# Kernel tuning notes

Hardware: AMD Instinct MI355X
Metric: run time of the kernel (lower is better)

## Reference

```python
import jax, jax.numpy as jnp
import numpy as np


def setup_inputs() -> dict:
    key = jax.random.key(0)
    ks = jax.random.split(key, 12)
    B, L, N, C, Ct, H, RH1, RH2, S = 64, 64, 256, 8, 4, 128, 128, 64, 4
    def rn(k, shape, s=0.08):
        return jax.random.normal(k, shape, dtype=jnp.float32) * s
    return dict(
        x=jax.random.normal(ks[0], (B, L, N, C * Ct), dtype=jnp.float32),
        hidden_intensity=jax.random.normal(ks[1], (B, N, H), dtype=jnp.float32),
        r=jax.random.normal(ks[2], (B, S), dtype=jnp.float32),
        W_ih=rn(ks[3], (4 * H, C)), W_hh=rn(ks[4], (4 * H, H)),
        b_ih=jnp.zeros((4 * H,), jnp.float32), b_hh=jnp.zeros((4 * H,), jnp.float32),
        W1=rn(ks[5], (RH1, 2 * H + 1)), b1=jnp.zeros((RH1,), jnp.float32),
        W2=rn(ks[6], (RH2, RH1)), b2=jnp.zeros((RH2,), jnp.float32),
        W3=rn(ks[7], (C, RH2)), b3=jnp.zeros((C,), jnp.float32),
        Wf=rn(ks[8], (1, C)), bf=jnp.zeros((1,), jnp.float32),
    )


def reference(x, hidden_intensity, r, W_ih, W_hh, b_ih, b_hh,
              W1, b1, W2, b2, W3, b3, Wf, bf):
    # Faithful to torch: nn.LSTM has batch_first=False but is fed (B, L, C),
    # so B is the sequence axis, L the batch axis, and lstm_out[:, -1, :]
    # writes predictions into that last column, so only x[:, -1] matters.
    B, L, N, _ = x.shape
    C = W_ih.shape[1]
    Ct = x.shape[3] // C
    H = W_hh.shape[1]

    def lstm_all_times(seq):  # seq: (T, Bb, C) -> hidden at every time (T, Bb, H)
        xp = jnp.einsum('tbc,gc->tbg', seq, W_ih) + b_ih + b_hh  # (T, Bb, 4H)
        def step(carry, xt):
            h, c = carry
            g = xt + h @ W_hh.T
            i, f, gg, o = jnp.split(g, 4, axis=-1)  # torch gate order i,f,g,o
            c = jax.nn.sigmoid(f) * c + jax.nn.sigmoid(i) * jnp.tanh(gg)
            h = jax.nn.sigmoid(o) * jnp.tanh(c)
            return (h, c), h
        z0 = jnp.zeros((seq.shape[1], H), seq.dtype)
        _, hs = jax.lax.scan(step, (z0, z0), xp)
        return hs

    hi = jnp.broadcast_to(hidden_intensity[:, :, None, :], (B, N, Ct, H))

    def roll(last_col, rj):  # last_col: (B, N, Ct, C), rj: (B,)
        hs = lstm_all_times(last_col.reshape(B, N * Ct, C)).reshape(B, N, Ct, H)
        rr = jnp.broadcast_to(rj[:, None, None, None], (B, N, Ct, 1))
        z = jnp.concatenate([hs, hi, rr], axis=-1)       # (B, N, Ct, 2H+1)
        h1 = jax.nn.relu(z @ W1.T + b1)
        h2 = jax.nn.relu(h1 @ W2.T + b2)
        pr = h2 @ W3.T + b3                              # (B, N, Ct, C)
        contrib = (jax.nn.relu(pr) @ Wf.T + bf)[..., 0].sum(axis=2)  # (B, N)
        return pr, contrib

    last0 = x[:, -1, :, :].reshape(B, N, Ct, C)
    _, preds = jax.lax.scan(roll, last0, r.T)  # (S, B, N)
    return jnp.transpose(preds, (1, 2, 0))     # (B, N, steps_ahead)
```

## Files before the change

kernel.cpp:

```cpp
#include <hip/hip_runtime.h>
#include <hip/hip_bf16.h>


typedef __attribute__((ext_vector_type(8))) _Float16 half8;
typedef __attribute__((ext_vector_type(4))) float f32x4;

#define MFMAH(a, b, c) __builtin_amdgcn_mfma_f32_16x16x32_f16(a, b, c, 0, 0, 0)

__device__ __forceinline__ float sigf(float x)   { return 1.0f / (1.0f + __expf(-x)); }
__device__ __forceinline__ float tanh_f(float x) { return 1.0f - 2.0f / (__expf(2.0f * x) + 1.0f); }

__global__ void prep_k(const float* __restrict__ hi,
                       const float* __restrict__ W1, const float* __restrict__ W2,
                       const float* __restrict__ W3, const float* __restrict__ W_hh,
                       const float* __restrict__ W_ih,
                       _Float16* __restrict__ hi16, _Float16* __restrict__ wp1,
                       _Float16* __restrict__ wp2, _Float16* __restrict__ wp3,
                       _Float16* __restrict__ wpB)
{
    int i = blockIdx.x * 256 + threadIdx.x;
    if (i < 262144) {
        int e = i * 8;
        half8 v;
#pragma unroll
        for (int k = 0; k < 8; ++k) v[k] = (_Float16)hi[e + k];
        *(half8*)(hi16 + e) = v;
        return;
    }
    i -= 262144;
    if (i < 36864) {
        int fragid = i >> 9, lj = i & 511;
        int kt = fragid >> 3, nt = fragid & 7;
        int l = lj >> 3, j = lj & 7;
        int klocal = (l >> 4) * 8 + j;
        int o = nt * 16 + (l & 15);
        float v;
        if (kt < 8)      v = W1[o * 257 + kt * 32 + klocal];
        else             v = (klocal == 0) ? W1[o * 257 + 256] : 0.0f;
        wp1[i] = (_Float16)v;
        return;
    }
    i -= 36864;
    if (i < 8192) {
        int fragid = i >> 9, lj = i & 511;
        int kt = fragid >> 2, nt = fragid & 3;
        int l = lj >> 3, j = lj & 7;
        int k = kt * 32 + (l >> 4) * 8 + j;
        int o = nt * 16 + (l & 15);
        wp2[i] = (_Float16)W2[o * 128 + k];
        return;
    }
    i -= 8192;
    if (i < 1024) {
        int kt = i >> 9, lj = i & 511;
        int l = lj >> 3, j = lj & 7;
        int k = kt * 32 + (l >> 4) * 8 + j;
        int c = l & 15;
        wp3[i] = (_Float16)((c < 8) ? W3[c * 64 + k] : 0.0f);
        return;
    }
    i -= 1024;
    if (i < 81920) {
        int frag = i >> 9, lj = i & 511;
        int kt = frag >> 5, ntile = frag & 31;
        int l = lj >> 3, j = lj & 7;
        int klocal = (l >> 4) * 8 + j;
        int col = ntile * 16 + (l & 15);
        float v;
        if (kt < 4) v = W_hh[col * 128 + kt * 32 + klocal];
        else        v = (klocal < 8) ? W_ih[col * 8 + klocal] : 0.0f;
        wpB[i] = (_Float16)v;
    }
}

__global__ __launch_bounds__(512, 2) void fused_k(
    const float* __restrict__ x, const _Float16* __restrict__ hi16,
    const float* __restrict__ r, const _Float16* __restrict__ wpB,
    const float* __restrict__ b_ih, const float* __restrict__ b_hh,
    const _Float16* __restrict__ wp1, const _Float16* __restrict__ wp2,
    const _Float16* __restrict__ wp3, const float* __restrict__ b1,
    const float* __restrict__ b2, const float* __restrict__ b3,
    const float* __restrict__ Wf, const float* __restrict__ bfp,
    float* __restrict__ out)
{
    __shared__ __align__(16) _Float16 zone[2][4][640];
    __shared__ __align__(16) _Float16 xz[64][32];
    __shared__ __align__(16) _Float16 hsL[256 * 130];
    __shared__ __align__(16) _Float16 h1L[128 * 132];
    __shared__ __align__(16) _Float16 h2L[128 * 68];

    const int t  = threadIdx.x;
    const int cg = t >> 6, l = t & 63;
    const int li = l & 15, lk = l >> 4;
    const int q0 = blockIdx.x * 4, nblk = blockIdx.x;

    const int gsrc[4] = {1, 0, 2, 3};
    half8 bw[4][5];
#pragma unroll
    for (int g = 0; g < 4; ++g)
#pragma unroll
        for (int kt = 0; kt < 5; ++kt) {
            bw[g][kt] = *(const half8*)(wpB + (size_t)(kt * 32 + gsrc[g] * 8 + cg) * 512 + l * 8);
            asm volatile("" : "+a"(bw[g][kt]));
        }
    f32x4 bs4[4];
#pragma unroll
    for (int g = 0; g < 4; ++g) {
        int gc = gsrc[g] * 128 + cg * 16 + li;
        float bv = b_ih[gc] + b_hh[gc];
        bs4[g] = (f32x4){bv, bv, bv, bv};
    }

    if (t < 256) {
        int step = t >> 2, tt = t & 3;
        const float* src = x + (size_t)step * 524288 + 63 * 8192 + (q0 + tt) * 8;
        half8 v;
#pragma unroll
        for (int k = 0; k < 8; ++k) v[k] = (_Float16)src[k];
        *(half8*)&xz[step][tt * 8] = v;
    }

    const int zpl  = cg >> 1;
    const int jl   = (cg & 1) * 16 + li;
    const int roff = (li & 12) * 40 + lk * 8;
    const int srow = lk * 4;
    const _Float16* xrd = &xz[0][(li >> 2) * 8];
    const f32x4 z4 = (f32x4){0.0f, 0.0f, 0.0f, 0.0f};

    for (int j = 0; j < 4; ++j) {
        for (int i = t; i < 1280; i += 512) ((uint*)zone)[i] = 0;
        float cc = 0.0f;
        __syncthreads();

        f32x4 accx[4];
        {
            half8 xa0 = *(const half8*)(xrd);
#pragma unroll
            for (int g = 0; g < 4; ++g)
                accx[g] = MFMAH(xa0, bw[g][4], bs4[g]);
        }

        auto dostep = [&](int step, int p) {
            const int pn = p ^ 1;
            half8 ah[4];
#pragma unroll
            for (int kt = 0; kt < 4; ++kt)
                ah[kt] = *(const half8*)&zone[p][kt][roff];

            __builtin_amdgcn_s_setprio(1);
            f32x4 a0[4], a1[4];
#pragma unroll
            for (int g = 0; g < 4; ++g) {
                a0[g] = MFMAH(ah[0], bw[g][0], accx[g]);
                a1[g] = MFMAH(ah[2], bw[g][2], z4);
            }
#pragma unroll
            for (int g = 0; g < 4; ++g) {
                a0[g] = MFMAH(ah[1], bw[g][1], a0[g]);
                a1[g] = MFMAH(ah[3], bw[g][3], a1[g]);
            }
            float pf = a0[0][0] + a1[0][0];
            float sf = sigf(pf);
            float pi = a0[1][0] + a1[1][0];
            float pg = a0[2][0] + a1[2][0];
            float po = a0[3][0] + a1[3][0];
            cc = sf * cc + sigf(pi) * tanh_f(pg);
            float hv = sigf(po) * tanh_f(cc);
            __builtin_amdgcn_s_setprio(0);
            _Float16 h16 = (_Float16)hv;
            zone[pn][zpl][srow * 40 + jl] = h16;
            hsL[(step * 4 + lk) * 130 + cg * 16 + li] = h16;
            asm volatile("s_waitcnt lgkmcnt(0)\n\ts_barrier" ::: "memory");

            half8 xn = *(const half8*)(xrd + ((step + 1) & 63) * 32);
#pragma unroll
            for (int g = 0; g < 4; ++g)
                accx[g] = MFMAH(xn, bw[g][4], bs4[g]);
        };
        for (int s2 = 0; s2 < 32; ++s2) {
            dostep(s2 * 2,     0);
            dostep(s2 * 2 + 1, 1);
        }

#pragma unroll 1
        for (int p = 0; p < 2; ++p) {
            f32x4 acc[8];
            {
                float bias = b1[cg * 16 + li];
#pragma unroll
                for (int m = 0; m < 8; ++m)
                    acc[m] = (f32x4){bias, bias, bias, bias};
            }
#pragma unroll
            for (int kt = 0; kt < 9; ++kt) {
                half8 bv = *(const half8*)(wp1 + (size_t)(kt * 8 + cg) * 512 + l * 8);
#pragma unroll
                for (int m = 0; m < 8; ++m) {
                    int Mg = p * 8 + m;
                    half8 av;
                    if (kt < 4) {
                        av = *(const half8*)&hsL[(Mg * 16 + li) * 130 + kt * 32 + lk * 8];
                    } else if (kt < 8) {
                        int b = Mg * 4 + (li >> 2);
                        av = *(const half8*)(hi16 + ((size_t)b * 256 + nblk) * 128
                                             + (kt - 4) * 32 + lk * 8);
                    } else {
                        int b = Mg * 4 + (li >> 2);
                        av = (half8){0, 0, 0, 0, 0, 0, 0, 0};
                        if (lk == 0) av[0] = (_Float16)r[b * 4 + j];
                    }
                    acc[m] = MFMAH(av, bv, acc[m]);
                }
            }
#pragma unroll
            for (int m = 0; m < 8; ++m)
#pragma unroll
                for (int reg = 0; reg < 4; ++reg) {
                    float v = fmaxf(acc[m][reg], 0.0f);
                    h1L[(m * 16 + lk * 4 + reg) * 132 + cg * 16 + li] = (_Float16)v;
                }
            __syncthreads();

            {
                const int n2 = cg & 3, mg0 = (cg >> 2) * 4;
                f32x4 acc2[4];
                float bias = b2[n2 * 16 + li];
#pragma unroll
                for (int mi = 0; mi < 4; ++mi)
                    acc2[mi] = (f32x4){bias, bias, bias, bias};
#pragma unroll
                for (int kt = 0; kt < 4; ++kt) {
                    half8 bv = *(const half8*)(wp2 + (size_t)(kt * 4 + n2) * 512 + l * 8);
#pragma unroll
                    for (int mi = 0; mi < 4; ++mi) {
                        int m = mg0 + mi;
                        half8 av = *(const half8*)&h1L[(m * 16 + li) * 132 + kt * 32 + lk * 8];
                        acc2[mi] = MFMAH(av, bv, acc2[mi]);
                    }
                }
#pragma unroll
                for (int mi = 0; mi < 4; ++mi)
#pragma unroll
                    for (int reg = 0; reg < 4; ++reg) {
                        float v = fmaxf(acc2[mi][reg], 0.0f);
                        h2L[((mg0 + mi) * 16 + lk * 4 + reg) * 68 + n2 * 16 + li] = (_Float16)v;
                    }
            }
            __syncthreads();

            {
                f32x4 acc3 = z4;
#pragma unroll
                for (int kt = 0; kt < 2; ++kt) {
                    half8 av = *(const half8*)&h2L[(cg * 16 + li) * 68 + kt * 32 + lk * 8];
                    half8 bv = *(const half8*)(wp3 + (size_t)kt * 512 + l * 8);
                    acc3 = MFMAH(av, bv, acc3);
                }
                const int Mg = p * 8 + cg;
                const int c = li;
                const float b3v = (c < 8) ? b3[c] : 0.0f;
                const float wfv = (c < 8) ? Wf[c] : 0.0f;
                const int b = Mg * 4 + lk;
                float fr[4];
#pragma unroll
                for (int reg = 0; reg < 4; ++reg) {
                    float pr = acc3[reg] + b3v;
                    if (c < 8) xz[b][reg * 8 + c] = (_Float16)pr;
                    fr[reg] = (c < 8) ? fmaxf(pr, 0.0f) * wfv : 0.0f;
                }
#pragma unroll
                for (int reg = 0; reg < 4; ++reg) {
                    fr[reg] += __shfl_xor(fr[reg], 1);
                    fr[reg] += __shfl_xor(fr[reg], 2);
                    fr[reg] += __shfl_xor(fr[reg], 4);
                }
                if (li == 0) {
                    float v = fr[0] + fr[1] + fr[2] + fr[3] + 4.0f * bfp[0];
                    out[((size_t)b * 256 + nblk) * 4 + j] = v;
                }
            }
            __syncthreads();
        }
    }
}

extern "C" void kernel_launch(void* const* d_in, const int* in_sizes, int n_in,
                              void* d_out, int out_size, void* d_ws, size_t ws_size,
                              hipStream_t stream)
{
    const float* x   = (const float*)d_in[0];
    const float* hi  = (const float*)d_in[1];
    const float* r   = (const float*)d_in[2];
    const float* Wih = (const float*)d_in[3];
    const float* Whh = (const float*)d_in[4];
    const float* bih = (const float*)d_in[5];
    const float* bhh = (const float*)d_in[6];
    const float* W1  = (const float*)d_in[7];
    const float* b1  = (const float*)d_in[8];
    const float* W2  = (const float*)d_in[9];
    const float* b2  = (const float*)d_in[10];
    const float* W3  = (const float*)d_in[11];
    const float* b3  = (const float*)d_in[12];
    const float* Wf  = (const float*)d_in[13];
    const float* bf  = (const float*)d_in[14];
    float* out = (float*)d_out;

    _Float16* hi16 = (_Float16*)d_ws;
    _Float16* wp1  = hi16 + 2097152;
    _Float16* wp2  = wp1 + 36864;
    _Float16* wp3  = wp2 + 8192;
    _Float16* wpB  = wp3 + 1024;

    prep_k<<<1524, 256, 0, stream>>>(hi, W1, W2, W3, Whh, Wih,
                                     hi16, wp1, wp2, wp3, wpB);
    fused_k<<<256, 512, 0, stream>>>(x, hi16, r, wpB, bih, bhh,
                                     wp1, wp2, wp3, b1, b2, b3, Wf, bf, out);
}
```

Measured before the change: 281.3 us.

## Wavefront-pipeline the four autoregressive rolls with per-timestep MLP fusion

Result: faster. 253.4 us (-9.9%).

```diff
diff --git a/kernel.cpp b/kernel.cpp
--- a/kernel.cpp
+++ b/kernel.cpp
@@ -84,15 +84,14 @@
     float* __restrict__ out)
 {
     __shared__ __align__(16) _Float16 zone[2][4][640];
-    __shared__ __align__(16) _Float16 xz[64][32];
-    __shared__ __align__(16) _Float16 hsL[256 * 130];
-    __shared__ __align__(16) _Float16 h1L[128 * 132];
-    __shared__ __align__(16) _Float16 h2L[128 * 68];
+    __shared__ __align__(16) _Float16 curA[4][64][32];
+    __shared__ __align__(16) _Float16 h1L[16 * 136];
+    __shared__ __align__(16) _Float16 h2L[16 * 72];
 
     const int t  = threadIdx.x;
     const int cg = t >> 6, l = t & 63;
     const int li = l & 15, lk = l >> 4;
-    const int q0 = blockIdx.x * 4, nblk = blockIdx.x;
+    const int nblk = blockIdx.x, q0 = nblk * 4;
 
     const int gsrc[4] = {1, 0, 2, 3};
     half8 bw[4][5];
@@ -111,176 +110,148 @@
         bs4[g] = (f32x4){bv, bv, bv, bv};
     }
 
+    for (int i = t; i < 2560; i += 512) ((uint*)zone)[i] = 0;
+    for (int i = t; i < 3072; i += 512) ((uint*)&curA[1][0][0])[i] = 0;
     if (t < 256) {
-        int step = t >> 2, tt = t & 3;
-        const float* src = x + (size_t)step * 524288 + 63 * 8192 + (q0 + tt) * 8;
+        int st = t >> 2, tt = t & 3;
+        const float* src = x + (size_t)st * 524288 + 63 * 8192 + (q0 + tt) * 8;
         half8 v;
 #pragma unroll
         for (int k = 0; k < 8; ++k) v[k] = (_Float16)src[k];
-        *(half8*)&xz[step][tt * 8] = v;
-    }
-
-    const int zpl  = cg >> 1;
-    const int jl   = (cg & 1) * 16 + li;
-    const int roff = (li & 12) * 40 + lk * 8;
-    const int srow = lk * 4;
-    const _Float16* xrd = &xz[0][(li >> 2) * 8];
+        *(half8*)&curA[0][st][tt * 8] = v;
+    }
+    float cc[4] = {0.0f, 0.0f, 0.0f, 0.0f};
+    __syncthreads();
+
     const f32x4 z4 = (f32x4){0.0f, 0.0f, 0.0f, 0.0f};
-
-    for (int j = 0; j < 4; ++j) {
-        for (int i = t; i < 1280; i += 512) ((uint*)zone)[i] = 0;
-        float cc = 0.0f;
-        __syncthreads();
-
-        f32x4 accx[4];
+    const int zpl = cg >> 1, jl = (cg & 1) * 16 + li;
+    const int roffL = li * 40 + lk * 8;
+    const int jx = li >> 2, sx = li & 3;
+    const float b1v = b1[cg * 16 + li];
+    const float b2v = (cg < 4) ? b2[cg * 16 + li] : 0.0f;
+    const float b3v = (li < 8) ? b3[li] : 0.0f;
+    const float wfv = (li < 8) ? Wf[li] : 0.0f;
+    const float bfv = bfp[0];
+
+#pragma unroll 1
+    for (int T = 0; T < 67; ++T) {
+        const int p = T & 1, pn = p ^ 1;
+        const int tb = (T - jx) & 63;
+
+        half8 xa = *(const half8*)&curA[jx][tb][sx * 8];
+        half8 ahi[4];
+#pragma unroll
+        for (int kt = 0; kt < 4; ++kt)
+            ahi[kt] = *(const half8*)(hi16 + ((size_t)(tb * 256 + nblk)) * 128
+                                      + kt * 32 + lk * 8);
+        half8 arf = (half8){0, 0, 0, 0, 0, 0, 0, 0};
+        if (lk == 0) arf[0] = (_Float16)r[tb * 4 + jx];
+
+        half8 ah[4];
+#pragma unroll
+        for (int kt = 0; kt < 4; ++kt)
+            ah[kt] = *(const half8*)&zone[p][kt][roffL];
+
+        f32x4 a0[4], a1[4];
+#pragma unroll
+        for (int g = 0; g < 4; ++g)
+            a0[g] = MFMAH(xa, bw[g][4], bs4[g]);
+#pragma unroll
+        for (int g = 0; g < 4; ++g) {
+            a0[g] = MFMAH(ah[0], bw[g][0], a0[g]);
+            a1[g] = MFMAH(ah[2], bw[g][2], z4);
+        }
+#pragma unroll
+        for (int g = 0; g < 4; ++g) {
+            a0[g] = MFMAH(ah[1], bw[g][1], a0[g]);
+            a1[g] = MFMAH(ah[3], bw[g][3], a1[g]);
+        }
+
+        const int troll = T - lk;
+        const bool act = (unsigned)troll < 64u;
+        _Float16 hw[4];
+#pragma unroll
+        for (int reg = 0; reg < 4; ++reg) {
+            float pf = a0[0][reg] + a1[0][reg];
+            float pi = a0[1][reg] + a1[1][reg];
+            float pg = a0[2][reg] + a1[2][reg];
+            float po = a0[3][reg] + a1[3][reg];
+            float ccp = (troll == 0) ? 0.0f : cc[reg];
+            float ncc = sigf(pf) * ccp + sigf(pi) * tanh_f(pg);
+            float hv  = sigf(po) * tanh_f(ncc);
+            cc[reg] = act ? ncc : 0.0f;
+            hw[reg] = act ? (_Float16)hv : (_Float16)0.0f;
+        }
+#pragma unroll
+        for (int reg = 0; reg < 4; ++reg)
+            zone[pn][zpl][(lk * 4 + reg) * 40 + jl] = hw[reg];
+        asm volatile("s_waitcnt lgkmcnt(0)\n\ts_barrier" ::: "memory");
+
+        f32x4 c0 = (f32x4){b1v, b1v, b1v, b1v}, c1 = z4;
+#pragma unroll
+        for (int kt = 0; kt < 4; ++kt) {
+            half8 az = *(const half8*)&zone[pn][kt][roffL];
+            half8 bv = *(const half8*)(wp1 + (size_t)(kt * 8 + cg) * 512 + l * 8);
+            c0 = MFMAH(az, bv, c0);
+            half8 bv2 = *(const half8*)(wp1 + (size_t)((kt + 4) * 8 + cg) * 512 + l * 8);
+            c1 = MFMAH(ahi[kt], bv2, c1);
+        }
         {
-            half8 xa0 = *(const half8*)(xrd);
-#pragma unroll
-            for (int g = 0; g < 4; ++g)
-                accx[g] = MFMAH(xa0, bw[g][4], bs4[g]);
-        }
-
-        auto dostep = [&](int step, int p) {
-            const int pn = p ^ 1;
-            half8 ah[4];
-#pragma unroll
-            for (int kt = 0; kt < 4; ++kt)
-                ah[kt] = *(const half8*)&zone[p][kt][roff];
-
-            __builtin_amdgcn_s_setprio(1);
-            f32x4 a0[4], a1[4];
-#pragma unroll
-            for (int g = 0; g < 4; ++g) {
-                a0[g] = MFMAH(ah[0], bw[g][0], accx[g]);
-                a1[g] = MFMAH(ah[2], bw[g][2], z4);
-            }
-#pragma unroll
-            for (int g = 0; g < 4; ++g) {
-                a0[g] = MFMAH(ah[1], bw[g][1], a0[g]);
-                a1[g] = MFMAH(ah[3], bw[g][3], a1[g]);
-            }
-            float pf = a0[0][0] + a1[0][0];
-            float sf = sigf(pf);
-            float pi = a0[1][0] + a1[1][0];
-            float pg = a0[2][0] + a1[2][0];
-            float po = a0[3][0] + a1[3][0];
-            cc = sf * cc + sigf(pi) * tanh_f(pg);
-            float hv = sigf(po) * tanh_f(cc);
-            __builtin_amdgcn_s_setprio(0);
-            _Float16 h16 = (_Float16)hv;
-            zone[pn][zpl][srow * 40 + jl] = h16;
-            hsL[(step * 4 + lk) * 130 + cg * 16 + li] = h16;
-            asm volatile("s_waitcnt lgkmcnt(0)\n\ts_barrier" ::: "memory");
-
-            half8 xn = *(const half8*)(xrd + ((step + 1) & 63) * 32);
-#pragma unroll
-            for (int g = 0; g < 4; ++g)
-                accx[g] = MFMAH(xn, bw[g][4], bs4[g]);
-        };
-        for (int s2 = 0; s2 < 32; ++s2) {
-            dostep(s2 * 2,     0);
-            dostep(s2 * 2 + 1, 1);
-        }
-
-#pragma unroll 1
-        for (int p = 0; p < 2; ++p) {
-            f32x4 acc[8];
-            {
-                float bias = b1[cg * 16 + li];
-#pragma unroll
-                for (int m = 0; m < 8; ++m)
-                    acc[m] = (f32x4){bias, bias, bias, bias};
-            }
-#pragma unroll
-            for (int kt = 0; kt < 9; ++kt) {
-                half8 bv = *(const half8*)(wp1 + (size_t)(kt * 8 + cg) * 512 + l * 8);
-#pragma unroll
-                for (int m = 0; m < 8; ++m) {
-                    int Mg = p * 8 + m;
-                    half8 av;
-                    if (kt < 4) {
-                        av = *(const half8*)&hsL[(Mg * 16 + li) * 130 + kt * 32 + lk * 8];
-                    } else if (kt < 8) {
-                        int b = Mg * 4 + (li >> 2);
-                        av = *(const half8*)(hi16 + ((size_t)b * 256 + nblk) * 128
-                                             + (kt - 4) * 32 + lk * 8);
-                    } else {
-                        int b = Mg * 4 + (li >> 2);
-                        av = (half8){0, 0, 0, 0, 0, 0, 0, 0};
-                        if (lk == 0) av[0] = (_Float16)r[b * 4 + j];
-                    }
-                    acc[m] = MFMAH(av, bv, acc[m]);
-                }
-            }
-#pragma unroll
-            for (int m = 0; m < 8; ++m)
-#pragma unroll
-                for (int reg = 0; reg < 4; ++reg) {
-                    float v = fmaxf(acc[m][reg], 0.0f);
-                    h1L[(m * 16 + lk * 4 + reg) * 132 + cg * 16 + li] = (_Float16)v;
-                }
-            __syncthreads();
-
-            {
-                const int n2 = cg & 3, mg0 = (cg >> 2) * 4;
-                f32x4 acc2[4];
-                float bias = b2[n2 * 16 + li];
-#pragma unroll
-                for (int mi = 0; mi < 4; ++mi)
-                    acc2[mi] = (f32x4){bias, bias, bias, bias};
-#pragma unroll
-                for (int kt = 0; kt < 4; ++kt) {
-                    half8 bv = *(const half8*)(wp2 + (size_t)(kt * 4 + n2) * 512 + l * 8);
-#pragma unroll
-                    for (int mi = 0; mi < 4; ++mi) {
-                        int m = mg0 + mi;
-                        half8 av = *(const half8*)&h1L[(m * 16 + li) * 132 + kt * 32 + lk * 8];
-                        acc2[mi] = MFMAH(av, bv, acc2[mi]);
-                    }
-                }
-#pragma unroll
-                for (int mi = 0; mi < 4; ++mi)
-#pragma unroll
-                    for (int reg = 0; reg < 4; ++reg) {
-                        float v = fmaxf(acc2[mi][reg], 0.0f);
-                        h2L[((mg0 + mi) * 16 + lk * 4 + reg) * 68 + n2 * 16 + li] = (_Float16)v;
-                    }
-            }
-            __syncthreads();
-
-            {
-                f32x4 acc3 = z4;
-#pragma unroll
-                for (int kt = 0; kt < 2; ++kt) {
-                    half8 av = *(const half8*)&h2L[(cg * 16 + li) * 68 + kt * 32 + lk * 8];
-                    half8 bv = *(const half8*)(wp3 + (size_t)kt * 512 + l * 8);
-                    acc3 = MFMAH(av, bv, acc3);
-                }
-                const int Mg = p * 8 + cg;
-                const int c = li;
-                const float b3v = (c < 8) ? b3[c] : 0.0f;
-                const float wfv = (c < 8) ? Wf[c] : 0.0f;
-                const int b = Mg * 4 + lk;
-                float fr[4];
-#pragma unroll
-                for (int reg = 0; reg < 4; ++reg) {
-                    float pr = acc3[reg] + b3v;
-                    if (c < 8) xz[b][reg * 8 + c] = (_Float16)pr;
-                    fr[reg] = (c < 8) ? fmaxf(pr, 0.0f) * wfv : 0.0f;
-                }
-#pragma unroll
-                for (int reg = 0; reg < 4; ++reg) {
-                    fr[reg] += __shfl_xor(fr[reg], 1);
-                    fr[reg] += __shfl_xor(fr[reg], 2);
-                    fr[reg] += __shfl_xor(fr[reg], 4);
-                }
-                if (li == 0) {
-                    float v = fr[0] + fr[1] + fr[2] + fr[3] + 4.0f * bfp[0];
-                    out[((size_t)b * 256 + nblk) * 4 + j] = v;
-                }
-            }
-            __syncthreads();
-        }
+            half8 bv = *(const half8*)(wp1 + (size_t)(8 * 8 + cg) * 512 + l * 8);
+            c1 = MFMAH(arf, bv, c1);
+        }
+#pragma unroll
+        for (int reg = 0; reg < 4; ++reg) {
+            float v = fmaxf(c0[reg] + c1[reg], 0.0f);
+            h1L[(lk * 4 + reg) * 136 + cg * 16 + li] = (_Float16)v;
+        }
+        asm volatile("s_waitcnt lgkmcnt(0)\n\ts_barrier" ::: "memory");
+
+        if (cg < 4) {
+            f32x4 d0 = (f32x4){b2v, b2v, b2v, b2v}, d1 = z4;
+#pragma unroll
+            for (int kt = 0; kt < 4; ++kt) {
+                half8 av = *(const half8*)&h1L[li * 136 + kt * 32 + lk * 8];
+                half8 bv = *(const half8*)(wp2 + (size_t)(kt * 4 + cg) * 512 + l * 8);
+                if (kt & 1) d1 = MFMAH(av, bv, d1);
+                else        d0 = MFMAH(av, bv, d0);
+            }
+#pragma unroll
+            for (int reg = 0; reg < 4; ++reg) {
+                float v = fmaxf(d0[reg] + d1[reg], 0.0f);
+                h2L[(lk * 4 + reg) * 72 + cg * 16 + li] = (_Float16)v;
+            }
+        }
+        asm volatile("s_waitcnt lgkmcnt(0)\n\ts_barrier" ::: "memory");
+
+        if (cg == 0) {
+            f32x4 e = z4;
+#pragma unroll
+            for (int kt = 0; kt < 2; ++kt) {
+                half8 av = *(const half8*)&h2L[li * 72 + kt * 32 + lk * 8];
+                half8 bv = *(const half8*)(wp3 + (size_t)kt * 512 + l * 8);
+                e = MFMAH(av, bv, e);
+            }
+            float fr[4];
+#pragma unroll
+            for (int reg = 0; reg < 4; ++reg) {
+                float pr = e[reg] + b3v;
+                if (act && lk < 3 && li < 8)
+                    curA[lk + 1][troll][reg * 8 + li] = (_Float16)pr;
+                fr[reg] = (act && li < 8) ? fmaxf(pr, 0.0f) * wfv : 0.0f;
+            }
+#pragma unroll
+            for (int reg = 0; reg < 4; ++reg) {
+                fr[reg] += __shfl_xor(fr[reg], 1);
+                fr[reg] += __shfl_xor(fr[reg], 2);
+                fr[reg] += __shfl_xor(fr[reg], 4);
+            }
+            if (li == 0 && act) {
+                float v = fr[0] + fr[1] + fr[2] + fr[3] + 4.0f * bfv;
+                out[((size_t)troll * 256 + nblk) * 4 + lk] = v;
+            }
+        }
+        asm volatile("s_waitcnt lgkmcnt(0)\n\ts_barrier" ::: "memory");
     }
 }
 
```
